# Performance work log

Hardware: AMD Instinct MI355X
Metric: run time of the kernel (lower is better)

## Reference

```python
import jax, jax.numpy as jnp
import numpy as np

B, S, D = 2, 2048, 1024
N_HEADS = 16
HEAD_DIM = D // N_HEADS


def setup_inputs() -> dict:
    key = jax.random.key(0)
    k1, k2, k3, k4, k5 = jax.random.split(key, 5)
    query = jax.random.normal(k1, (B, S, D), dtype=jnp.float32)
    key_t = jax.random.normal(k2, (B, S, D), dtype=jnp.float32)
    value = jax.random.normal(k3, (B, S, D), dtype=jnp.float32)
    # nn.Linear(dim, 3*dim): weight [3D, D], bias [3D]
    lim = 1.0 / np.sqrt(D)
    W_qkv_w = jax.random.uniform(k4, (3 * D, D), dtype=jnp.float32, minval=-lim, maxval=lim)
    W_qkv_b = jax.random.uniform(k5, (3 * D,), dtype=jnp.float32, minval=-lim, maxval=lim)
    return {"query": query, "key": key_t, "value": value, "W_qkv_w": W_qkv_w, "W_qkv_b": W_qkv_b}


def reference(query, key, value, W_qkv_w, W_qkv_b):
    # key/value args are ignored by the original module: Q, K, V all come
    # from the fused projection of `query` (faithful to source).
    b, s, d = query.shape
    qkv = query @ W_qkv_w.T + W_qkv_b                      # [B, S, 3D]
    qkv = qkv.reshape(b, s, 3, N_HEADS, HEAD_DIM)
    qkv = jnp.transpose(qkv, (2, 0, 3, 1, 4))              # [3, B, H, S, dh]
    q, k, v = qkv[0], qkv[1], qkv[2]
    # Faithful (inverted) scaling: scores DIVIDED by sqrt(1/d_model)
    scale_factor = jnp.sqrt(jnp.asarray(1.0 / (HEAD_DIM * N_HEADS), dtype=query.dtype))
    scores = jnp.einsum('bhqd,bhkd->bhqk', q, k) / scale_factor
    attn = jax.nn.softmax(scores, axis=-1)                 # dropout p=0.0 -> identity
    out = jnp.einsum('bhqk,bhkd->bhqd', attn, v)           # [B, H, S, dh]
    out = jnp.transpose(out, (0, 2, 1, 3)).reshape(b, s, d)
    return out
```

## Files before the change

kernel.cpp:

```cpp
#include <hip/hip_runtime.h>

#define B_  2
#define S_  2048
#define D_  1024
#define H_  16
#define DH_ 64
#define BH_ (B_*H_)
#define NT_ (S_/64)

using f32x4   = __attribute__((ext_vector_type(4))) float;
using short4v = __attribute__((ext_vector_type(4))) short;
using short8v = __attribute__((ext_vector_type(8))) short;

__device__ short g_qh[(size_t)BH_*S_*DH_];
__device__ short g_ql[(size_t)BH_*S_*DH_];
__device__ short g_kh[(size_t)BH_*S_*DH_];
__device__ short g_kl[(size_t)BH_*S_*DH_];
__device__ short g_vt[(size_t)BH_*DH_*S_];

__device__ __forceinline__ short f2bf(float x){
  unsigned u = __builtin_bit_cast(unsigned, x);
  u += 0x7fffu + ((u >> 16) & 1u);
  return (short)(unsigned short)(u >> 16);
}
__device__ __forceinline__ float bf2f(short h){
  return __builtin_bit_cast(float, ((unsigned)(unsigned short)h) << 16);
}
__device__ __forceinline__ void split4f(const float4 v, short4v& h4, short4v& l4){
  float f[4] = {v.x, v.y, v.z, v.w};
#pragma unroll
  for (int i = 0; i < 4; ++i){
    short hh = f2bf(f[i]);
    h4[i] = hh;
    l4[i] = f2bf(f[i] - bf2f(hh));
  }
}

#define MFMA16(A,B,C) __builtin_amdgcn_mfma_f32_16x16x32_bf16((A),(B),(C),0,0,0)

__global__ __launch_bounds__(256) void qkv_proj_mfma(
    const float* __restrict__ X, const float* __restrict__ W,
    const float* __restrict__ bias)
{
  __shared__ short AH[128][40], AL[128][40], BHs[128][40], BLs[128][40];

  const int tid = threadIdx.x;
  const int w  = tid >> 6;
  const int ln = tid & 15;
  const int g  = (tid & 63) >> 4;
  const int wr = w >> 1, wc = w & 1;
  const int m0 = blockIdx.y * 128;
  const int n0 = blockIdx.x * 128;
  const int which = n0 >> 10;

  f32x4 zero4 = {0.f, 0.f, 0.f, 0.f};
  f32x4 acc[4][4];
#pragma unroll
  for (int mf = 0; mf < 4; ++mf)
#pragma unroll
    for (int nf = 0; nf < 4; ++nf) acc[mf][nf] = zero4;

  for (int k0 = 0; k0 < D_; k0 += 32) {
#pragma unroll
    for (int rep = 0; rep < 4; ++rep) {
      int idx = rep * 256 + tid;
      int r  = idx >> 3;
      int c4 = (idx & 7) << 2;
      float4 a = *(const float4*)&X[(size_t)(m0 + r) * D_ + k0 + c4];
      float4 b = *(const float4*)&W[(size_t)(n0 + r) * D_ + k0 + c4];
      short4v ah4, al4, bh4, bl4;
      split4f(a, ah4, al4);
      split4f(b, bh4, bl4);
      *(short4v*)&AH [r][c4] = ah4;
      *(short4v*)&BHs[r][c4] = bh4;
      if (which < 2) {
        *(short4v*)&AL [r][c4] = al4;
        *(short4v*)&BLs[r][c4] = bl4;
      }
    }
    __syncthreads();

    short8v ah[4], al[4], bhf[4], blf[4];
#pragma unroll
    for (int mf = 0; mf < 4; ++mf) {
      ah[mf] = *(const short8v*)&AH[64*wr + 16*mf + ln][8*g];
      if (which < 2) al[mf] = *(const short8v*)&AL[64*wr + 16*mf + ln][8*g];
    }
#pragma unroll
    for (int nf = 0; nf < 4; ++nf) {
      bhf[nf] = *(const short8v*)&BHs[64*wc + 16*nf + ln][8*g];
      if (which < 2) blf[nf] = *(const short8v*)&BLs[64*wc + 16*nf + ln][8*g];
    }
#pragma unroll
    for (int mf = 0; mf < 4; ++mf)
#pragma unroll
      for (int nf = 0; nf < 4; ++nf) {
        acc[mf][nf] = MFMA16(ah[mf], bhf[nf], acc[mf][nf]);
        if (which < 2) {
          acc[mf][nf] = MFMA16(al[mf], bhf[nf], acc[mf][nf]);
          acc[mf][nf] = MFMA16(ah[mf], blf[nf], acc[mf][nf]);
        }
      }
    __syncthreads();
  }

#pragma unroll
  for (int nf = 0; nf < 4; ++nf) {
    int col = n0 + 64*wc + 16*nf + ln;
    float bb = bias[col];
    int hh = (col & 1023) >> 6;
    int dh = col & 63;
#pragma unroll
    for (int mf = 0; mf < 4; ++mf) {
      int row0 = m0 + 64*wr + 16*mf + 4*g;
      int bidx = row0 >> 11;
      int s0   = row0 & 2047;
      int bh   = bidx * H_ + hh;
      if (which == 2) {
        short4v v4;
#pragma unroll
        for (int i = 0; i < 4; ++i) v4[i] = f2bf(acc[mf][nf][i] + bb);
        *(short4v*)&g_vt[((size_t)bh * DH_ + dh) * S_ + s0] = v4;
      } else {
        short* dH = (which == 0) ? g_qh : g_kh;
        short* dL = (which == 0) ? g_ql : g_kl;
        float sc  = (which == 0) ? 32.0f : 1.0f;
#pragma unroll
        for (int i = 0; i < 4; ++i) {
          float v = (acc[mf][nf][i] + bb) * sc;
          short hi = f2bf(v);
          short lo = f2bf(v - bf2f(hi));
          size_t o = ((size_t)bh * S_ + s0 + i) * DH_ + dh;
          dH[o] = hi;
          dL[o] = lo;
        }
      }
    }
  }
}

__global__ __launch_bounds__(256, 2) void attn_mfma(float* __restrict__ out)
{
  __shared__ short PS[4][32][64];

  const int tid = threadIdx.x;
  const int w  = tid >> 6;
  const int ln = tid & 15;
  const int g  = (tid & 63) >> 4;

  const int bid = blockIdx.x;
  const int swz = (bid & 7) * 64 + (bid >> 3);
  const int bh  = swz >> 4;
  const int q0  = (swz & 15) * 128;
  const int b   = bh >> 4, h = bh & 15;

  const size_t qb = (size_t)bh * S_ * DH_;
  const short* __restrict__ Kh = g_kh + qb;
  const short* __restrict__ Kl = g_kl + qb;
  const short* __restrict__ Vt = g_vt + (size_t)bh * DH_ * S_;

  short8v qh[2][2], ql[2][2];
#pragma unroll
  for (int rf = 0; rf < 2; ++rf)
#pragma unroll
    for (int ks = 0; ks < 2; ++ks) {
      size_t o = qb + (size_t)(q0 + 32*w + 16*rf + ln) * DH_ + 32*ks + 8*g;
      qh[rf][ks] = *(const short8v*)&g_qh[o];
      ql[rf][ks] = *(const short8v*)&g_ql[o];
    }

  f32x4 zero4 = {0.f,0.f,0.f,0.f};
  f32x4 o_[2][4];
  float m_[2][4], l_[2][4];
#pragma unroll
  for (int rf = 0; rf < 2; ++rf)
#pragma unroll
    for (int i = 0; i < 4; ++i) {
      o_[rf][i&3] = o_[rf][i&3];
    }
#pragma unroll
  for (int rf = 0; rf < 2; ++rf)
#pragma unroll
    for (int nf = 0; nf < 4; ++nf) o_[rf][nf] = zero4;
#pragma unroll
  for (int rf = 0; rf < 2; ++rf)
#pragma unroll
    for (int i = 0; i < 4; ++i) { m_[rf][i] = -1e30f; l_[rf][i] = 0.f; }

  for (int t = 0; t < NT_; ++t) {
    const int t0 = t * 64;

    short8v kh[2][4], kl[2][4];
#pragma unroll
    for (int ks = 0; ks < 2; ++ks)
#pragma unroll
      for (int nf = 0; nf < 4; ++nf) {
        size_t o = (size_t)(t0 + 16*nf + ln) * DH_ + 32*ks + 8*g;
        kh[ks][nf] = *(const short8v*)&Kh[o];
        kl[ks][nf] = *(const short8v*)&Kl[o];
      }

    f32x4 s[2][4];
#pragma unroll
    for (int rf = 0; rf < 2; ++rf)
#pragma unroll
      for (int nf = 0; nf < 4; ++nf) s[rf][nf] = zero4;
#pragma unroll
    for (int rf = 0; rf < 2; ++rf)
#pragma unroll
      for (int ks = 0; ks < 2; ++ks)
#pragma unroll
        for (int nf = 0; nf < 4; ++nf) {
          s[rf][nf] = MFMA16(qh[rf][ks], kh[ks][nf], s[rf][nf]);
          s[rf][nf] = MFMA16(ql[rf][ks], kh[ks][nf], s[rf][nf]);
          s[rf][nf] = MFMA16(qh[rf][ks], kl[ks][nf], s[rf][nf]);
        }

    short8v vb[2][4];
#pragma unroll
    for (int ks = 0; ks < 2; ++ks)
#pragma unroll
      for (int nf = 0; nf < 4; ++nf)
        vb[ks][nf] = *(const short8v*)&Vt[(size_t)(16*nf + ln) * S_ + t0 + 32*ks + 8*g];

#pragma unroll
    for (int rf = 0; rf < 2; ++rf)
#pragma unroll
      for (int i = 0; i < 4; ++i) {
        float mt = fmaxf(fmaxf(s[rf][0][i], s[rf][1][i]),
                         fmaxf(s[rf][2][i], s[rf][3][i]));
        mt = fmaxf(mt, __shfl_xor(mt, 1));
        mt = fmaxf(mt, __shfl_xor(mt, 2));
        mt = fmaxf(mt, __shfl_xor(mt, 4));
        mt = fmaxf(mt, __shfl_xor(mt, 8));
        float mn = fmaxf(m_[rf][i], mt);
        float corr = __expf(m_[rf][i] - mn);
        float sum = 0.f;
#pragma unroll
        for (int nf = 0; nf < 4; ++nf) {
          float p = __expf(s[rf][nf][i] - mn);
          sum += p;
          s[rf][nf][i] = p;
        }
        sum += __shfl_xor(sum, 1);
        sum += __shfl_xor(sum, 2);
        sum += __shfl_xor(sum, 4);
        sum += __shfl_xor(sum, 8);
        l_[rf][i] = l_[rf][i] * corr + sum;
        m_[rf][i] = mn;
        const int row = 16*rf + 4*g + i;
        const int e   = (4*g + i) & 7;
#pragma unroll
        for (int nf = 0; nf < 4; ++nf) {
          o_[rf][nf][i] *= corr;
          PS[w][row][(16*nf + ln) ^ (e << 3)] = f2bf(s[rf][nf][i]);
        }
      }

#pragma unroll
    for (int rf = 0; rf < 2; ++rf)
#pragma unroll
      for (int ks = 0; ks < 2; ++ks) {
        const short8v pa =
            *(const short8v*)&PS[w][16*rf + ln][(32*ks + 8*g) ^ ((ln & 7) << 3)];
#pragma unroll
        for (int nf = 0; nf < 4; ++nf)
          o_[rf][nf] = MFMA16(pa, vb[ks][nf], o_[rf][nf]);
      }
  }

#pragma unroll
  for (int rf = 0; rf < 2; ++rf)
#pragma unroll
    for (int i = 0; i < 4; ++i) {
      float inv = 1.0f / l_[rf][i];
      int row = q0 + 32*w + 16*rf + 4*g + i;
      float* op = &out[((size_t)b * S_ + row) * D_ + h * DH_];
#pragma unroll
      for (int nf = 0; nf < 4; ++nf)
        op[16*nf + ln] = o_[rf][nf][i] * inv;
    }
}

extern "C" void kernel_launch(void* const* d_in, const int* in_sizes, int n_in,
                              void* d_out, int out_size, void* d_ws, size_t ws_size,
                              hipStream_t stream) {
    (void)d_ws; (void)ws_size; (void)n_in; (void)in_sizes;
    const float* X    = (const float*)d_in[0];
    const float* W    = (const float*)d_in[3];
    const float* bias = (const float*)d_in[4];
    float* out = (float*)d_out;

    dim3 gProj(24, 32);
    qkv_proj_mfma<<<gProj, 256, 0, stream>>>(X, W, bias);

    attn_mfma<<<dim3(512), 256, 0, stream>>>(out);
}
```

Measured before the change: 347.3 us.

## Prefetch QKV projection tiles into registers and stage epilogue stores through LDS

The projection kernel now loads the next K-slice of X and W into registers while the current slice's MFMAs run, hiding global load latency behind compute. The epilogue stages results in a shared-memory tile so that Q/K hi/lo and transposed V are written with coalesced 16-byte stores instead of scattered 2-byte or 8-byte stores. This costs extra registers for the prefetch buffers, plus extra barriers and shared-memory traffic in the epilogue. A dead self-assignment loop in the attention kernel is also removed.

```diff
diff --git a/kernel.cpp b/kernel.cpp
--- a/kernel.cpp
+++ b/kernel.cpp
@@ -42,7 +42,12 @@
     const float* __restrict__ X, const float* __restrict__ W,
     const float* __restrict__ bias)
 {
-  __shared__ short AH[128][40], AL[128][40], BHs[128][40], BLs[128][40];
+  __shared__ short SM[20480];
+  short (*AH )[40] = (short(*)[40])(SM);
+  short (*AL )[40] = (short(*)[40])(SM + 5120);
+  short (*BHs)[40] = (short(*)[40])(SM + 10240);
+  short (*BLs)[40] = (short(*)[40])(SM + 15360);
+  short *LT = SM;
 
   const int tid = threadIdx.x;
   const int w  = tid >> 6;
@@ -60,17 +65,25 @@
 #pragma unroll
     for (int nf = 0; nf < 4; ++nf) acc[mf][nf] = zero4;
 
+  float4 xa[4], wb[4];
+#pragma unroll
+  for (int rep = 0; rep < 4; ++rep) {
+    int idx = rep * 256 + tid;
+    int r  = idx >> 3;
+    int c4 = (idx & 7) << 2;
+    xa[rep] = *(const float4*)&X[(size_t)(m0 + r) * D_ + c4];
+    wb[rep] = *(const float4*)&W[(size_t)(n0 + r) * D_ + c4];
+  }
+
   for (int k0 = 0; k0 < D_; k0 += 32) {
 #pragma unroll
     for (int rep = 0; rep < 4; ++rep) {
       int idx = rep * 256 + tid;
       int r  = idx >> 3;
       int c4 = (idx & 7) << 2;
-      float4 a = *(const float4*)&X[(size_t)(m0 + r) * D_ + k0 + c4];
-      float4 b = *(const float4*)&W[(size_t)(n0 + r) * D_ + k0 + c4];
       short4v ah4, al4, bh4, bl4;
-      split4f(a, ah4, al4);
-      split4f(b, bh4, bl4);
+      split4f(xa[rep], ah4, al4);
+      split4f(wb[rep], bh4, bl4);
       *(short4v*)&AH [r][c4] = ah4;
       *(short4v*)&BHs[r][c4] = bh4;
       if (which < 2) {
@@ -80,6 +93,17 @@
     }
     __syncthreads();
 
+    if (k0 + 32 < D_) {
+#pragma unroll
+      for (int rep = 0; rep < 4; ++rep) {
+        int idx = rep * 256 + tid;
+        int r  = idx >> 3;
+        int c4 = (idx & 7) << 2;
+        xa[rep] = *(const float4*)&X[(size_t)(m0 + r) * D_ + k0 + 32 + c4];
+        wb[rep] = *(const float4*)&W[(size_t)(n0 + r) * D_ + k0 + 32 + c4];
+      }
+    }
+
     short8v ah[4], al[4], bhf[4], blf[4];
 #pragma unroll
     for (int mf = 0; mf < 4; ++mf) {
@@ -104,37 +128,91 @@
     __syncthreads();
   }
 
-#pragma unroll
-  for (int nf = 0; nf < 4; ++nf) {
-    int col = n0 + 64*wc + 16*nf + ln;
-    float bb = bias[col];
-    int hh = (col & 1023) >> 6;
-    int dh = col & 63;
-#pragma unroll
-    for (int mf = 0; mf < 4; ++mf) {
-      int row0 = m0 + 64*wr + 16*mf + 4*g;
-      int bidx = row0 >> 11;
-      int s0   = row0 & 2047;
-      int bh   = bidx * H_ + hh;
-      if (which == 2) {
+  const float sc = (which == 0) ? 32.0f : 1.0f;
+  float bb[4];
+#pragma unroll
+  for (int nf = 0; nf < 4; ++nf) bb[nf] = bias[n0 + 64*wc + 16*nf + ln];
+#pragma unroll
+  for (int mf = 0; mf < 4; ++mf)
+#pragma unroll
+    for (int nf = 0; nf < 4; ++nf)
+#pragma unroll
+      for (int i = 0; i < 4; ++i)
+        acc[mf][nf][i] = (acc[mf][nf][i] + bb[nf]) * sc;
+
+  const int bidx  = m0 >> 11;
+  const int s0    = m0 & 2047;
+  const int hbase = (n0 & 1023) >> 6;
+
+  if (which == 2) {
+#pragma unroll
+    for (int nf = 0; nf < 4; ++nf) {
+      int dl = 64*wc + 16*nf + ln;
+#pragma unroll
+      for (int mf = 0; mf < 4; ++mf) {
+        int sl = 64*wr + 16*mf + 4*g;
         short4v v4;
 #pragma unroll
-        for (int i = 0; i < 4; ++i) v4[i] = f2bf(acc[mf][nf][i] + bb);
-        *(short4v*)&g_vt[((size_t)bh * DH_ + dh) * S_ + s0] = v4;
-      } else {
-        short* dH = (which == 0) ? g_qh : g_kh;
-        short* dL = (which == 0) ? g_ql : g_kl;
-        float sc  = (which == 0) ? 32.0f : 1.0f;
+        for (int i = 0; i < 4; ++i) v4[i] = f2bf(acc[mf][nf][i]);
+        *(short4v*)&LT[dl*136 + sl] = v4;
+      }
+    }
+    __syncthreads();
+#pragma unroll
+    for (int rep = 0; rep < 8; ++rep) {
+      int idx = rep * 256 + tid;
+      int r  = idx >> 4;
+      int sg = idx & 15;
+      short8v v = *(const short8v*)&LT[r*136 + sg*8];
+      int h = hbase + (r >> 6), dh = r & 63;
+      *(short8v*)&g_vt[(((size_t)(bidx*H_ + h))*DH_ + dh)*S_ + s0 + sg*8] = v;
+    }
+  } else {
+    short* dH = (which == 0) ? g_qh : g_kh;
+    short* dL = (which == 0) ? g_ql : g_kl;
+#pragma unroll
+    for (int mf = 0; mf < 4; ++mf)
+#pragma unroll
+      for (int nf = 0; nf < 4; ++nf) {
+        int dl = 64*wc + 16*nf + ln;
+#pragma unroll
+        for (int i = 0; i < 4; ++i)
+          LT[(64*wr + 16*mf + 4*g + i)*136 + dl] = f2bf(acc[mf][nf][i]);
+      }
+    __syncthreads();
+#pragma unroll
+    for (int rep = 0; rep < 8; ++rep) {
+      int idx = rep * 256 + tid;
+      int r  = idx >> 4;
+      int sg = idx & 15;
+      short8v v = *(const short8v*)&LT[r*136 + sg*8];
+      int h = hbase + (sg >> 3);
+      int dh = (sg & 7) * 8;
+      *(short8v*)&dH[(((size_t)(bidx*H_ + h))*S_ + s0 + r)*DH_ + dh] = v;
+    }
+    __syncthreads();
+#pragma unroll
+    for (int mf = 0; mf < 4; ++mf)
+#pragma unroll
+      for (int nf = 0; nf < 4; ++nf) {
+        int dl = 64*wc + 16*nf + ln;
 #pragma unroll
         for (int i = 0; i < 4; ++i) {
-          float v = (acc[mf][nf][i] + bb) * sc;
+          float v = acc[mf][nf][i];
           short hi = f2bf(v);
-          short lo = f2bf(v - bf2f(hi));
-          size_t o = ((size_t)bh * S_ + s0 + i) * DH_ + dh;
-          dH[o] = hi;
-          dL[o] = lo;
-        }
-      }
+          LT[(64*wr + 16*mf + 4*g + i)*136 + dl] = f2bf(v - bf2f(hi));
+        }
+      }
+    __syncthreads();
+#pragma unroll
+    for (int rep = 0; rep < 8; ++rep) {
+      int idx = rep * 256 + tid;
+      int r  = idx >> 4;
+      int sg = idx & 15;
+      short8v v = *(const short8v*)&LT[r*136 + sg*8];
+      int h = hbase + (sg >> 3);
+      int dh = (sg & 7) * 8;
+      *(short8v*)&dL[(((size_t)(bidx*H_ + h))*S_ + s0 + r)*DH_ + dh] = v;
     }
   }
 }
@@ -172,12 +250,6 @@
   f32x4 zero4 = {0.f,0.f,0.f,0.f};
   f32x4 o_[2][4];
   float m_[2][4], l_[2][4];
-#pragma unroll
-  for (int rf = 0; rf < 2; ++rf)
-#pragma unroll
-    for (int i = 0; i < 4; ++i) {
-      o_[rf][i&3] = o_[rf][i&3];
-    }
 #pragma unroll
   for (int rf = 0; rf < 2; ++rf)
 #pragma unroll
```

New measurement: 318.3 us. 8.3% less time.
